# Kernel tuning notes

Measured on AMD Instinct MI355X. Metric: run time of the kernel, lower is better.

Reference implementation:

```python
import jax, jax.numpy as jnp
import numpy as np

B, D_IN, UNITS, H = 512, 1024, 1024, 8
K = V = UNITS // H  # key_dim = value_dim = head_dim = 128
P = 2 * H * K + H * V + 2 * H + UNITS  # total projection size = 4112


def setup_inputs() -> dict:
    key = jax.random.key(0)
    ks = jax.random.split(key, 7)
    return {
        "inputs": jax.random.normal(ks[0], (B, D_IN), jnp.float32),
        "h_tm1": jax.random.normal(ks[1], (B, UNITS), jnp.float32),
        "C_tm1": jax.random.normal(ks[2], (B, H * K * V), jnp.float32),
        "n_tm1": jax.random.uniform(ks[3], (B, H * K), jnp.float32),
        "kernel": jax.random.normal(ks[4], (D_IN, P), jnp.float32) / np.sqrt(D_IN),
        "recurrent_kernel": jax.random.normal(ks[5], (UNITS, P), jnp.float32) / np.sqrt(UNITS),
        "bias": jnp.zeros((P,), jnp.float32),
    }


def reference(inputs, h_tm1, C_tm1, n_tm1, kernel, recurrent_kernel, bias):
    b = inputs.shape[0]
    # fused input + recurrent projection: (b, P)
    proj = inputs @ kernel + bias + h_tm1 @ recurrent_kernel
    qs = H * K
    q = proj[:, :qs].reshape(b, H, K)
    k = proj[:, qs:2 * qs].reshape(b, H, K)
    v = proj[:, 2 * qs:2 * qs + H * V].reshape(b, H, V)
    i_g = jnp.exp(proj[:, 2 * qs + H * V:2 * qs + H * V + H])        # (b, H) exponential input gate
    f_g = jax.nn.sigmoid(proj[:, 2 * qs + H * V + H:2 * qs + H * V + 2 * H])  # (b, H)
    o_g = jax.nn.sigmoid(proj[:, -UNITS:])                            # (b, units)
    C = C_tm1.reshape(b, H, K, V)
    n = n_tm1.reshape(b, H, K)
    # covariance update: C_t = f*C + i*(k outer v)  -> (b, H, K, V)
    C_t = f_g[:, :, None, None] * C + i_g[:, :, None, None] * jnp.einsum('bhk,bhv->bhkv', k, v)
    # normalizer update: n_t = f*n + i*k
    n_t = f_g[:, :, None] * n + i_g[:, :, None] * k
    # readout: (C_t^T q) / (n_t . q)
    retr = jnp.einsum('bhkv,bhk->bhv', C_t, q)
    denom = jnp.sum(n_t * q, axis=-1, keepdims=True) + 1e-8
    h_t = o_g * (retr / denom).reshape(b, H * V)
    return h_t, C_t.reshape(b, H * K * V), n_t.reshape(b, H * K)
```

## Files before the change

kernel.cpp:

```cpp
#include <hip/hip_runtime.h>
#include <hip/hip_fp16.h>
#include <math.h>

#define NPROJ 4112
#define HOFF  0
#define COFF  524288
#define NOFF  67633152
#define SLICE 2105344
#define WTROWS 4160

using f16x8 = __attribute__((ext_vector_type(8))) _Float16;
using f32x4 = __attribute__((ext_vector_type(4))) float;

typedef __attribute__((address_space(1))) const ushort gu16;
typedef __attribute__((address_space(3))) ushort lu16;

#define ASCALE 64.0f
#define PSCALE (1.0 / 4096.0)

__device__ __forceinline__ void fp16_split(float x, ushort& h, ushort& l)
{
    const __half h1 = __float2half(x);
    h = __half_as_ushort(h1);
    l = __half_as_ushort(__float2half(x - __half2float(h1)));
}

__global__ __launch_bounds__(256)
void split_a2(const float* __restrict__ X0, const float* __restrict__ X1,
              ushort* __restrict__ Ah, ushort* __restrict__ Al)
{
    const int idx8 = (blockIdx.x * 256 + threadIdx.x) << 3;
    const int row = idx8 >> 11, k = idx8 & 2047;
    const float* src = (k < 1024) ? (X0 + (size_t)row * 1024 + k)
                                  : (X1 + (size_t)row * 1024 + (k - 1024));
    const float4 v0 = *(const float4*)src;
    const float4 v1 = *(const float4*)(src + 4);
    const float vv[8] = {v0.x, v0.y, v0.z, v0.w, v1.x, v1.y, v1.z, v1.w};
    ushort hh[8], ll[8];
#pragma unroll
    for (int i = 0; i < 8; ++i) fp16_split(vv[i] * ASCALE, hh[i], ll[i]);
    uint4 uh, ul;
    uh.x = hh[0] | ((unsigned)hh[1] << 16); uh.y = hh[2] | ((unsigned)hh[3] << 16);
    uh.z = hh[4] | ((unsigned)hh[5] << 16); uh.w = hh[6] | ((unsigned)hh[7] << 16);
    ul.x = ll[0] | ((unsigned)ll[1] << 16); ul.y = ll[2] | ((unsigned)ll[3] << 16);
    ul.z = ll[4] | ((unsigned)ll[5] << 16); ul.w = ll[6] | ((unsigned)ll[7] << 16);
    *(uint4*)(Ah + idx8) = uh;
    *(uint4*)(Al + idx8) = ul;
}

__global__ __launch_bounds__(256)
void split_w2(const float* __restrict__ W0, const float* __restrict__ W1,
              ushort* __restrict__ Wh, ushort* __restrict__ Wl)
{
    __shared__ __align__(16) ushort Th[64][72];
    __shared__ __align__(16) ushort Tl[64][72];
    const int t = threadIdx.x;
    const int kcat0 = blockIdx.x * 64;
    const int n0    = blockIdx.y * 64;
    const float* __restrict__ W = (kcat0 < 1024) ? W0 : W1;
    const int kbase = kcat0 & 1023;
    const int kr = t >> 4;
    const int nc = (t & 15) << 2;
    const bool ok = (n0 + nc) < NPROJ;
#pragma unroll
    for (int ii = 0; ii < 4; ++ii) {
        const int kl = kr + ii * 16;
        float4 w = make_float4(0.f, 0.f, 0.f, 0.f);
        if (ok) w = *(const float4*)(W + (size_t)(kbase + kl) * NPROJ + n0 + nc);
        const float x[4] = {w.x, w.y, w.z, w.w};
#pragma unroll
        for (int c = 0; c < 4; ++c) {
            ushort hh, ll;
            fp16_split(x[c] * ASCALE, hh, ll);
            Th[nc + c][kl] = hh;
            Tl[nc + c][kl] = ll;
        }
    }
    __syncthreads();
#pragma unroll
    for (int p = 0; p < 2; ++p) {
        const int c  = t + (p << 8);
        const int nn = c >> 3;
        const int kq = (c & 7) << 3;
        *(uint4*)(Wh + (size_t)(n0 + nn) * 2048 + kcat0 + kq) = *(uint4*)&Th[nn][kq];
        *(uint4*)(Wl + (size_t)(n0 + nn) * 2048 + kcat0 + kq) = *(uint4*)&Tl[nn][kq];
    }
}

__global__ __launch_bounds__(256)
void proj_mfma2(const ushort* __restrict__ Ah, const ushort* __restrict__ Al,
                const ushort* __restrict__ Wh, const ushort* __restrict__ Wl,
                float* __restrict__ pbuf)
{
    __shared__ __align__(16) ushort As[2][4096];
    __shared__ __align__(16) ushort Bs[2][4096];

    const int t    = threadIdx.x;
    const int col0 = blockIdx.x * 64;
    const int row0 = blockIdx.y * 64;
    const int z    = blockIdx.z;
    const int lane = t & 63, wid = t >> 6;
    const int wr = wid >> 1, wc = wid & 1;
    const int lr = lane & 15, lq = lane >> 4;

    const int r0s = t >> 3,        ch0 = t & 7;
    const int r1s = r0s + 32;
    const int so0 = (ch0 ^ (r0s & 7)) << 3;
    const int so1 = (ch0 ^ (r1s & 7)) << 3;
    const size_t kb = (size_t)z << 10;
    const size_t arow0 = (size_t)(row0 + r0s) * 2048 + kb;
    const size_t arow1 = (size_t)(row0 + r1s) * 2048 + kb;
    const size_t brow0 = (size_t)(col0 + r0s) * 2048 + kb;
    const size_t brow1 = (size_t)(col0 + r1s) * 2048 + kb;
    const int d0 = t << 3;
    const int d1 = d0 + 2048;

    int aoff[2][2], boff[2][2];
#pragma unroll
    for (int mi = 0; mi < 2; ++mi)
#pragma unroll
        for (int kh = 0; kh < 2; ++kh) {
            const int ra = (wr << 5) + (mi << 4) + lr;
            aoff[mi][kh] = ra * 64 + ((((kh << 2) + lq) ^ (ra & 7)) << 3);
            const int rb = (wc << 5) + (mi << 4) + lr;
            boff[mi][kh] = rb * 64 + ((((kh << 2) + lq) ^ (rb & 7)) << 3);
        }

    f32x4 acc[2][2] = {};

    for (int kt = 0; kt < 16; ++kt) {
        const int ko = kt << 6;
        __builtin_amdgcn_global_load_lds((gu16*)(Ah + arow0 + ko + so0), (lu16*)&As[0][d0], 16, 0, 0);
        __builtin_amdgcn_global_load_lds((gu16*)(Ah + arow1 + ko + so1), (lu16*)&As[0][d1], 16, 0, 0);
        __builtin_amdgcn_global_load_lds((gu16*)(Al + arow0 + ko + so0), (lu16*)&As[1][d0], 16, 0, 0);
        __builtin_amdgcn_global_load_lds((gu16*)(Al + arow1 + ko + so1), (lu16*)&As[1][d1], 16, 0, 0);
        __builtin_amdgcn_global_load_lds((gu16*)(Wh + brow0 + ko + so0), (lu16*)&Bs[0][d0], 16, 0, 0);
        __builtin_amdgcn_global_load_lds((gu16*)(Wh + brow1 + ko + so1), (lu16*)&Bs[0][d1], 16, 0, 0);
        __builtin_amdgcn_global_load_lds((gu16*)(Wl + brow0 + ko + so0), (lu16*)&Bs[1][d0], 16, 0, 0);
        __builtin_amdgcn_global_load_lds((gu16*)(Wl + brow1 + ko + so1), (lu16*)&Bs[1][d1], 16, 0, 0);
        __syncthreads();

#pragma unroll
        for (int kh = 0; kh < 2; ++kh) {
            f16x8 ah[2], al[2], bh[2], bl[2];
#pragma unroll
            for (int mi = 0; mi < 2; ++mi) {
                ah[mi] = *(const f16x8*)&As[0][aoff[mi][kh]];
                al[mi] = *(const f16x8*)&As[1][aoff[mi][kh]];
                bh[mi] = *(const f16x8*)&Bs[0][boff[mi][kh]];
                bl[mi] = *(const f16x8*)&Bs[1][boff[mi][kh]];
            }
#pragma unroll
            for (int mi = 0; mi < 2; ++mi)
#pragma unroll
                for (int ni = 0; ni < 2; ++ni) {
                    acc[mi][ni] = __builtin_amdgcn_mfma_f32_16x16x32_f16(ah[mi], bh[ni], acc[mi][ni], 0, 0, 0);
                    acc[mi][ni] = __builtin_amdgcn_mfma_f32_16x16x32_f16(ah[mi], bl[ni], acc[mi][ni], 0, 0, 0);
                    acc[mi][ni] = __builtin_amdgcn_mfma_f32_16x16x32_f16(al[mi], bh[ni], acc[mi][ni], 0, 0, 0);
                    acc[mi][ni] = __builtin_amdgcn_mfma_f32_16x16x32_f16(al[mi], bl[ni], acc[mi][ni], 0, 0, 0);
                }
        }
        __syncthreads();
    }

    float* __restrict__ dst = pbuf + (size_t)z * SLICE;
#pragma unroll
    for (int mi = 0; mi < 2; ++mi) {
        const int row = row0 + (wr << 5) + (mi << 4) + (lq << 2);
#pragma unroll
        for (int ni = 0; ni < 2; ++ni) {
            const int col = col0 + (wc << 5) + (ni << 4) + lr;
            if (col < NPROJ) {
#pragma unroll
                for (int j = 0; j < 4; ++j)
                    dst[(size_t)(row + j) * NPROJ + col] = acc[mi][ni][j];
            }
        }
    }
}

template<int NS>
__device__ __forceinline__ double psumN(const float* __restrict__ pb, size_t off,
                                        double pscale, float bv)
{
    double s = 0.0;
#pragma unroll
    for (int i = 0; i < NS; ++i) s += (double)pb[off + (size_t)i * SLICE];
    return s * pscale + (double)bv;
}

template<int NS>
__global__ __launch_bounds__(256)
void mlstm_update_fused(const float* __restrict__ pbuf, const float* __restrict__ bias,
                        const float* __restrict__ C_tm1, const float* __restrict__ n_tm1,
                        float* __restrict__ out, double pscale)
{
    const int bh = blockIdx.x;
    const int b  = bh >> 3;
    const int h  = bh & 7;
    const int t  = threadIdx.x;
    const size_t pb = (size_t)b * NPROJ;

    __shared__ double q_s[128];
    __shared__ double coef_s[128];
    __shared__ double prod_s[128];
    __shared__ double red_s[8][128];
    __shared__ double denom_s;

    const double ig = exp(psumN<NS>(pbuf, pb + 3072 + h, pscale, bias[3072 + h]));
    const double fg = 1.0 / (1.0 + exp(-psumN<NS>(pbuf, pb + 3080 + h, pscale, bias[3080 + h])));

    if (t < 128) {
        const double qv = psumN<NS>(pbuf, pb + h * 128 + t, pscale, bias[h * 128 + t]);
        const double kv = psumN<NS>(pbuf, pb + 1024 + h * 128 + t, pscale, bias[1024 + h * 128 + t]);
        q_s[t] = qv;
        const double cf = ig * kv;
        coef_s[t] = cf;
        const double nv = fma(fg, (double)n_tm1[(size_t)b * 1024 + h * 128 + t], cf);
        out[NOFF + (size_t)b * 1024 + h * 128 + t] = (float)nv;
        prod_s[t] = nv * qv;
    }
    __syncthreads();

    const int g = t >> 5;
    const int s = t & 31;
    const float4* __restrict__ Cin  = (const float4*)(C_tm1 + (size_t)bh * 16384);
    float4*       __restrict__ Cout = (float4*)(out + COFF + (size_t)bh * 16384);
    double v0, v1, v2, v3;
    {
        const size_t vo = pb + 2048 + h * 128 + (s << 2);
        const int    vb = 2048 + h * 128 + (s << 2);
        v0 = psumN<NS>(pbuf, vo + 0, pscale, bias[vb + 0]);
        v1 = psumN<NS>(pbuf, vo + 1, pscale, bias[vb + 1]);
        v2 = psumN<NS>(pbuf, vo + 2, pscale, bias[vb + 2]);
        v3 = psumN<NS>(pbuf, vo + 3, pscale, bias[vb + 3]);
    }

    double r0 = 0.0, r1 = 0.0, r2 = 0.0, r3 = 0.0;
#pragma unroll 4
    for (int it = 0; it < 16; ++it) {
        const int kr = (it << 3) + g;
        const float4 cc = Cin[(kr << 5) + s];
        const double cf = coef_s[kr];
        const double qv = q_s[kr];
        const double c0 = fma(fg, (double)cc.x, cf * v0);
        const double c1 = fma(fg, (double)cc.y, cf * v1);
        const double c2 = fma(fg, (double)cc.z, cf * v2);
        const double c3 = fma(fg, (double)cc.w, cf * v3);
        float4 cn;
        cn.x = (float)c0; cn.y = (float)c1; cn.z = (float)c2; cn.w = (float)c3;
        Cout[(kr << 5) + s] = cn;
        r0 = fma(c0, qv, r0);
        r1 = fma(c1, qv, r1);
        r2 = fma(c2, qv, r2);
        r3 = fma(c3, qv, r3);
    }
    red_s[g][(s << 2) + 0] = r0;
    red_s[g][(s << 2) + 1] = r1;
    red_s[g][(s << 2) + 2] = r2;
    red_s[g][(s << 2) + 3] = r3;
    __syncthreads();

    if (t < 64) {
        double x = prod_s[t] + prod_s[t + 64];
#pragma unroll
        for (int off = 32; off > 0; off >>= 1) x += __shfl_xor(x, off, 64);
        if (t == 0) denom_s = x + 1e-8;
    }
    __syncthreads();

    if (t < 32) {
        double r[4] = {0.0, 0.0, 0.0, 0.0};
#pragma unroll
        for (int gg = 0; gg < 8; ++gg) {
#pragma unroll
            for (int j = 0; j < 4; ++j) r[j] += red_s[gg][(t << 2) + j];
        }
        const double inv = 1.0 / denom_s;
        const size_t oo = pb + 3088 + h * 128 + (t << 2);
        const int    ob = 3088 + h * 128 + (t << 2);
        float4 hv;
        hv.x = (float)((1.0 / (1.0 + exp(-psumN<NS>(pbuf, oo + 0, pscale, bias[ob + 0])))) * (r[0] * inv));
        hv.y = (float)((1.0 / (1.0 + exp(-psumN<NS>(pbuf, oo + 1, pscale, bias[ob + 1])))) * (r[1] * inv));
        hv.z = (float)((1.0 / (1.0 + exp(-psumN<NS>(pbuf, oo + 2, pscale, bias[ob + 2])))) * (r[2] * inv));
        hv.w = (float)((1.0 / (1.0 + exp(-psumN<NS>(pbuf, oo + 3, pscale, bias[ob + 3])))) * (r[3] * inv));
        *(float4*)(out + HOFF + (size_t)b * 1024 + h * 128 + (t << 2)) = hv;
    }
}

__global__ __launch_bounds__(256)
void proj_gemm_sk(const float* __restrict__ X0, const float* __restrict__ X1,
                  const float* __restrict__ W0, const float* __restrict__ W1,
                  float* __restrict__ pbuf)
{
    const int K = 1024;
    const int N = NPROJ;
    __shared__ float As[32][68];
    __shared__ float Bs[32][68];

    const int tid  = threadIdx.x;
    const int row0 = blockIdx.y * 64;
    const int col0 = blockIdx.x * 64;
    const int z    = blockIdx.z;
    const float* __restrict__ A = (z < 2) ? X0 : X1;
    const float* __restrict__ W = (z < 2) ? W0 : W1;
    const int kbase = (z & 1) << 9;
    const int tx = tid & 15, ty = tid >> 4;

    const int ar = tid >> 2;
    const int aq = (tid & 3) << 2;
    const int bk = tid >> 4;
    const int bn = (tid & 15) << 2;
    const int gn = (col0 + bn < N) ? (col0 + bn) : (N - 4);
    const float* __restrict__ arow = A + (size_t)(row0 + ar) * K;

    float  acc32[4][4];
    double acc64[4][4];
#pragma unroll
    for (int i = 0; i < 4; ++i)
#pragma unroll
        for (int j = 0; j < 4; ++j) { acc32[i][j] = 0.f; acc64[i][j] = 0.0; }

    float4 pa0 = *(const float4*)(arow + kbase + aq);
    float4 pa1 = *(const float4*)(arow + kbase + aq + 16);
    float4 pb0 = *(const float4*)(W + (size_t)(kbase + bk) * N + gn);
    float4 pb1 = *(const float4*)(W + (size_t)(kbase + bk + 16) * N + gn);

    for (int kt = 0; kt < 16; ++kt) {
        As[aq + 0][ar] = pa0.x; As[aq + 1][ar] = pa0.y;
        As[aq + 2][ar] = pa0.z; As[aq + 3][ar] = pa0.w;
        As[aq + 16][ar] = pa1.x; As[aq + 17][ar] = pa1.y;
        As[aq + 18][ar] = pa1.z; As[aq + 19][ar] = pa1.w;
        *(float4*)&Bs[bk][bn]      = pb0;
        *(float4*)&Bs[bk + 16][bn] = pb1;
        __syncthreads();

        if (kt + 1 < 16) {
            const int k0n = kbase + ((kt + 1) << 5);
            pa0 = *(const float4*)(arow + k0n + aq);
            pa1 = *(const float4*)(arow + k0n + aq + 16);
            pb0 = *(const float4*)(W + (size_t)(k0n + bk) * N + gn);
            pb1 = *(const float4*)(W + (size_t)(k0n + bk + 16) * N + gn);
        }

#pragma unroll
        for (int kk = 0; kk < 32; ++kk) {
            const float4 av = *(const float4*)&As[kk][ty << 2];
            const float4 bv = *(const float4*)&Bs[kk][tx << 2];
            const float aa[4] = {av.x, av.y, av.z, av.w};
            const float bb[4] = {bv.x, bv.y, bv.z, bv.w};
#pragma unroll
            for (int i = 0; i < 4; ++i)
#pragma unroll
                for (int j = 0; j < 4; ++j)
                    acc32[i][j] = fmaf(aa[i], bb[j], acc32[i][j]);
        }
#pragma unroll
        for (int i = 0; i < 4; ++i)
#pragma unroll
            for (int j = 0; j < 4; ++j) {
                acc64[i][j] += (double)acc32[i][j];
                acc32[i][j] = 0.f;
            }
        __syncthreads();
    }

    float* __restrict__ dst = pbuf + (size_t)z * SLICE;
    const int c = col0 + (tx << 2);
    if (c < N) {
#pragma unroll
        for (int i = 0; i < 4; ++i) {
            const int row = row0 + (ty << 2) + i;
            float4 w;
            w.x = (float)acc64[i][0];
            w.y = (float)acc64[i][1];
            w.z = (float)acc64[i][2];
            w.w = (float)acc64[i][3];
            *(float4*)(dst + (size_t)row * N + c) = w;
        }
    }
}

__global__ __launch_bounds__(256)
void proj_gemm_fp32(const float* __restrict__ X0, const float* __restrict__ X1,
                    const float* __restrict__ W0, const float* __restrict__ W1,
                    const float* __restrict__ bias, float* __restrict__ proj)
{
    const int N = NPROJ;
    const int K = 1024;
    __shared__ float As[16][68];
    __shared__ float Bs[16][68];
    const int tid  = threadIdx.x;
    const int row0 = blockIdx.y * 64;
    const int col0 = blockIdx.x * 64;
    const int tx   = tid & 15;
    const int ty   = tid >> 4;
    float  acc32[4][4];
    double acc64[4][4];
#pragma unroll
    for (int i = 0; i < 4; ++i)
#pragma unroll
        for (int j = 0; j < 4; ++j) { acc32[i][j] = 0.f; acc64[i][j] = 0.0; }
    for (int src = 0; src < 2; ++src) {
        const float* __restrict__ A = src ? X1 : X0;
        const float* __restrict__ W = src ? W1 : W0;
        for (int kt = 0; kt < 64; ++kt) {
            const int k0 = kt << 4;
            {
                const int r  = tid >> 2;
                const int kq = (tid & 3) << 2;
                const float4 a = *(const float4*)(A + (size_t)(row0 + r) * K + k0 + kq);
                As[kq + 0][r] = a.x; As[kq + 1][r] = a.y;
                As[kq + 2][r] = a.z; As[kq + 3][r] = a.w;
            }
            {
                const int kr = tid >> 4;
                const int nc = (tid & 15) << 2;
                const int gn = col0 + nc;
                float4 bv = make_float4(0.f, 0.f, 0.f, 0.f);
                if (gn < N) bv = *(const float4*)(W + (size_t)(k0 + kr) * N + gn);
                *(float4*)&Bs[kr][nc] = bv;
            }
            __syncthreads();
#pragma unroll
            for (int kk = 0; kk < 16; ++kk) {
                const float4 av = *(const float4*)&As[kk][ty << 2];
                const float4 bv = *(const float4*)&Bs[kk][tx << 2];
                const float aa[4] = {av.x, av.y, av.z, av.w};
                const float bb[4] = {bv.x, bv.y, bv.z, bv.w};
#pragma unroll
                for (int i = 0; i < 4; ++i)
#pragma unroll
                    for (int j = 0; j < 4; ++j)
                        acc32[i][j] = fmaf(aa[i], bb[j], acc32[i][j]);
            }
            __syncthreads();
            if (kt & 1) {
#pragma unroll
                for (int i = 0; i < 4; ++i)
#pragma unroll
                    for (int j = 0; j < 4; ++j) {
                        acc64[i][j] += (double)acc32[i][j];
                        acc32[i][j] = 0.f;
                    }
            }
        }
    }
    const int c = col0 + (tx << 2);
    if (c < N) {
#pragma unroll
        for (int i = 0; i < 4; ++i) {
            const int row = row0 + (ty << 2) + i;
            float4 w;
            w.x = (float)(acc64[i][0] + (double)bias[c + 0]);
            w.y = (float)(acc64[i][1] + (double)bias[c + 1]);
            w.z = (float)(acc64[i][2] + (double)bias[c + 2]);
            w.w = (float)(acc64[i][3] + (double)bias[c + 3]);
            *(float4*)(proj + (size_t)row * N + c) = w;
        }
    }
}

__global__ __launch_bounds__(256)
void mlstm_update(const float* __restrict__ proj, const float* __restrict__ C_tm1,
                  const float* __restrict__ n_tm1, float* __restrict__ out)
{
    const int bh = blockIdx.x;
    const int b  = bh >> 3;
    const int h  = bh & 7;
    const int t  = threadIdx.x;
    const float* __restrict__ pr = proj + (size_t)b * NPROJ;

    __shared__ double q_s[128];
    __shared__ double coef_s[128];
    __shared__ double prod_s[128];
    __shared__ double red_s[8][128];
    __shared__ double denom_s;

    const double ig = exp((double)pr[3072 + h]);
    const double fg = 1.0 / (1.0 + exp(-(double)pr[3080 + h]));

    if (t < 128) {
        const double qv = (double)pr[h * 128 + t];
        const double kv = (double)pr[1024 + h * 128 + t];
        q_s[t] = qv;
        const double cf = ig * kv;
        coef_s[t] = cf;
        const double nv = fma(fg, (double)n_tm1[(size_t)b * 1024 + h * 128 + t], cf);
        out[NOFF + (size_t)b * 1024 + h * 128 + t] = (float)nv;
        prod_s[t] = nv * qv;
    }
    __syncthreads();

    const int g = t >> 5;
    const int s = t & 31;
    const float4* __restrict__ Cin  = (const float4*)(C_tm1 + (size_t)bh * 16384);
    float4*       __restrict__ Cout = (float4*)(out + COFF + (size_t)bh * 16384);
    const float4 vf = *(const float4*)(pr + 2048 + h * 128 + (s << 2));
    const double v0 = (double)vf.x, v1 = (double)vf.y, v2 = (double)vf.z, v3 = (double)vf.w;

    double r0 = 0.0, r1 = 0.0, r2 = 0.0, r3 = 0.0;
#pragma unroll 4
    for (int it = 0; it < 16; ++it) {
        const int kr = (it << 3) + g;
        const float4 cc = Cin[(kr << 5) + s];
        const double cf = coef_s[kr];
        const double qv = q_s[kr];
        const double c0 = fma(fg, (double)cc.x, cf * v0);
        const double c1 = fma(fg, (double)cc.y, cf * v1);
        const double c2 = fma(fg, (double)cc.z, cf * v2);
        const double c3 = fma(fg, (double)cc.w, cf * v3);
        float4 cn;
        cn.x = (float)c0; cn.y = (float)c1; cn.z = (float)c2; cn.w = (float)c3;
        Cout[(kr << 5) + s] = cn;
        r0 = fma(c0, qv, r0);
        r1 = fma(c1, qv, r1);
        r2 = fma(c2, qv, r2);
        r3 = fma(c3, qv, r3);
    }
    red_s[g][(s << 2) + 0] = r0;
    red_s[g][(s << 2) + 1] = r1;
    red_s[g][(s << 2) + 2] = r2;
    red_s[g][(s << 2) + 3] = r3;
    __syncthreads();

    if (t < 64) {
        double x = prod_s[t] + prod_s[t + 64];
#pragma unroll
        for (int off = 32; off > 0; off >>= 1) x += __shfl_xor(x, off, 64);
        if (t == 0) denom_s = x + 1e-8;
    }
    __syncthreads();

    if (t < 32) {
        double r[4] = {0.0, 0.0, 0.0, 0.0};
#pragma unroll
        for (int gg = 0; gg < 8; ++gg) {
#pragma unroll
            for (int j = 0; j < 4; ++j) r[j] += red_s[gg][(t << 2) + j];
        }
        const double inv = 1.0 / denom_s;
        const float* oo = pr + 3088 + h * 128 + (t << 2);
        float4 hv;
        hv.x = (float)((1.0 / (1.0 + exp(-(double)oo[0]))) * (r[0] * inv));
        hv.y = (float)((1.0 / (1.0 + exp(-(double)oo[1]))) * (r[1] * inv));
        hv.z = (float)((1.0 / (1.0 + exp(-(double)oo[2]))) * (r[2] * inv));
        hv.w = (float)((1.0 / (1.0 + exp(-(double)oo[3]))) * (r[3] * inv));
        *(float4*)(out + HOFF + (size_t)b * 1024 + h * 128 + (t << 2)) = hv;
    }
}

extern "C" void kernel_launch(void* const* d_in, const int* in_sizes, int n_in,
                              void* d_out, int out_size, void* d_ws, size_t ws_size,
                              hipStream_t stream)
{
    const float* inputs  = (const float*)d_in[0];
    const float* h_tm1   = (const float*)d_in[1];
    const float* C_tm1   = (const float*)d_in[2];
    const float* n_tm1   = (const float*)d_in[3];
    const float* kernelW = (const float*)d_in[4];
    const float* rkernel = (const float*)d_in[5];
    const float* bias    = (const float*)d_in[6];
    float* out = (float*)d_out;

    const size_t SZ_PB2 = (size_t)2 * SLICE * 4;
    const size_t SZ_A   = (size_t)512 * 2048 * 2;
    const size_t SZ_WT  = (size_t)WTROWS * 2048 * 2;
    const size_t OFF_AH = SZ_PB2;
    const size_t OFF_AL = OFF_AH + SZ_A;
    const size_t OFF_WH = OFF_AL + SZ_A;
    const size_t OFF_WL = OFF_WH + SZ_WT;
    const size_t NEED_MAIN = OFF_WL + SZ_WT;
    const size_t NEED_SK   = (size_t)4 * SLICE * 4;
    const size_t NEED_MIN  = (size_t)SLICE * 4;

    if (ws_size >= NEED_MAIN) {
        float*  pbuf = (float*)d_ws;
        ushort* Ah = (ushort*)((char*)d_ws + OFF_AH);
        ushort* Al = (ushort*)((char*)d_ws + OFF_AL);
        ushort* Wh = (ushort*)((char*)d_ws + OFF_WH);
        ushort* Wl = (ushort*)((char*)d_ws + OFF_WL);
        split_a2<<<dim3(512), dim3(256), 0, stream>>>(inputs, h_tm1, Ah, Al);
        split_w2<<<dim3(32, 65), dim3(256), 0, stream>>>(kernelW, rkernel, Wh, Wl);
        proj_mfma2<<<dim3(65, 8, 2), dim3(256), 0, stream>>>(Ah, Al, Wh, Wl, pbuf);
        mlstm_update_fused<2><<<dim3(4096), dim3(256), 0, stream>>>(pbuf, bias, C_tm1, n_tm1, out, PSCALE);
    } else if (ws_size >= NEED_SK) {
        float* pbuf = (float*)d_ws;
        proj_gemm_sk<<<dim3(65, 8, 4), dim3(256), 0, stream>>>(inputs, h_tm1, kernelW, rkernel, pbuf);
        mlstm_update_fused<4><<<dim3(4096), dim3(256), 0, stream>>>(pbuf, bias, C_tm1, n_tm1, out, 1.0);
    } else if (ws_size >= NEED_MIN) {
        float* proj = (float*)d_ws;
        proj_gemm_fp32<<<dim3(65, 8), dim3(256), 0, stream>>>(inputs, h_tm1, kernelW, rkernel, bias, proj);
        mlstm_update<<<dim3(4096), dim3(256), 0, stream>>>(proj, C_tm1, n_tm1, out);
    }
}
```

Baseline: 183.2 us.

## Double-buffer projection GEMM tiles, shrink K-step, drop low-low split product

```diff
diff --git a/kernel.cpp b/kernel.cpp
--- a/kernel.cpp
+++ b/kernel.cpp
@@ -88,7 +88,7 @@
 }
 
 __global__ __launch_bounds__(256)
-void proj_mfma2(const ushort* __restrict__ Ah, const ushort* __restrict__ Al,
+void proj_mfma3(const ushort* __restrict__ Ah, const ushort* __restrict__ Al,
                 const ushort* __restrict__ Wh, const ushort* __restrict__ Wl,
                 float* __restrict__ pbuf)
 {
@@ -103,65 +103,59 @@
     const int wr = wid >> 1, wc = wid & 1;
     const int lr = lane & 15, lq = lane >> 4;
 
-    const int r0s = t >> 3,        ch0 = t & 7;
-    const int r1s = r0s + 32;
-    const int so0 = (ch0 ^ (r0s & 7)) << 3;
-    const int so1 = (ch0 ^ (r1s & 7)) << 3;
+    const int rs = t >> 2, js = t & 3;
+    const int cs = (js + (rs >> 1)) & 3;
     const size_t kb = (size_t)z << 10;
-    const size_t arow0 = (size_t)(row0 + r0s) * 2048 + kb;
-    const size_t arow1 = (size_t)(row0 + r1s) * 2048 + kb;
-    const size_t brow0 = (size_t)(col0 + r0s) * 2048 + kb;
-    const size_t brow1 = (size_t)(col0 + r1s) * 2048 + kb;
-    const int d0 = t << 3;
-    const int d1 = d0 + 2048;
-
-    int aoff[2][2], boff[2][2];
-#pragma unroll
-    for (int mi = 0; mi < 2; ++mi)
-#pragma unroll
-        for (int kh = 0; kh < 2; ++kh) {
-            const int ra = (wr << 5) + (mi << 4) + lr;
-            aoff[mi][kh] = ra * 64 + ((((kh << 2) + lq) ^ (ra & 7)) << 3);
-            const int rb = (wc << 5) + (mi << 4) + lr;
-            boff[mi][kh] = rb * 64 + ((((kh << 2) + lq) ^ (rb & 7)) << 3);
-        }
+    const size_t arow = (size_t)(row0 + rs) * 2048 + kb + (cs << 3);
+    const size_t brow = (size_t)(col0 + rs) * 2048 + kb + (cs << 3);
+    const int d0 = t << 3, d1 = d0 + 2048;
+
+#define STG(BUF, KT)                                                                         \
+    {                                                                                        \
+        const int ko = (KT) << 5;                                                            \
+        __builtin_amdgcn_global_load_lds((gu16*)(Ah + arow + ko), (lu16*)&As[BUF][d0], 16, 0, 0); \
+        __builtin_amdgcn_global_load_lds((gu16*)(Al + arow + ko), (lu16*)&As[BUF][d1], 16, 0, 0); \
+        __builtin_amdgcn_global_load_lds((gu16*)(Wh + brow + ko), (lu16*)&Bs[BUF][d0], 16, 0, 0); \
+        __builtin_amdgcn_global_load_lds((gu16*)(Wl + brow + ko), (lu16*)&Bs[BUF][d1], 16, 0, 0); \
+    }
+
+    int aoff[2], boff[2];
+#pragma unroll
+    for (int mi = 0; mi < 2; ++mi) {
+        const int ra = (wr << 5) + (mi << 4) + lr;
+        aoff[mi] = (ra << 5) + (((lq - (ra >> 1)) & 3) << 3);
+        const int rb = (wc << 5) + (mi << 4) + lr;
+        boff[mi] = (rb << 5) + (((lq - (rb >> 1)) & 3) << 3);
+    }
 
     f32x4 acc[2][2] = {};
 
-    for (int kt = 0; kt < 16; ++kt) {
-        const int ko = kt << 6;
-        __builtin_amdgcn_global_load_lds((gu16*)(Ah + arow0 + ko + so0), (lu16*)&As[0][d0], 16, 0, 0);
-        __builtin_amdgcn_global_load_lds((gu16*)(Ah + arow1 + ko + so1), (lu16*)&As[0][d1], 16, 0, 0);
-        __builtin_amdgcn_global_load_lds((gu16*)(Al + arow0 + ko + so0), (lu16*)&As[1][d0], 16, 0, 0);
-        __builtin_amdgcn_global_load_lds((gu16*)(Al + arow1 + ko + so1), (lu16*)&As[1][d1], 16, 0, 0);
-        __builtin_amdgcn_global_load_lds((gu16*)(Wh + brow0 + ko + so0), (lu16*)&Bs[0][d0], 16, 0, 0);
-        __builtin_amdgcn_global_load_lds((gu16*)(Wh + brow1 + ko + so1), (lu16*)&Bs[0][d1], 16, 0, 0);
-        __builtin_amdgcn_global_load_lds((gu16*)(Wl + brow0 + ko + so0), (lu16*)&Bs[1][d0], 16, 0, 0);
-        __builtin_amdgcn_global_load_lds((gu16*)(Wl + brow1 + ko + so1), (lu16*)&Bs[1][d1], 16, 0, 0);
+    STG(0, 0)
+    __syncthreads();
+
+    for (int kt = 0; kt < 32; ++kt) {
+        const int cur = kt & 1;
+        if (kt + 1 < 32) STG(cur ^ 1, kt + 1)
+
+        f16x8 ah[2], al[2], bh[2], bl[2];
+#pragma unroll
+        for (int mi = 0; mi < 2; ++mi) {
+            ah[mi] = *(const f16x8*)&As[cur][aoff[mi]];
+            al[mi] = *(const f16x8*)&As[cur][2048 + aoff[mi]];
+            bh[mi] = *(const f16x8*)&Bs[cur][boff[mi]];
+            bl[mi] = *(const f16x8*)&Bs[cur][2048 + boff[mi]];
+        }
+#pragma unroll
+        for (int mi = 0; mi < 2; ++mi)
+#pragma unroll
+            for (int ni = 0; ni < 2; ++ni) {
+                acc[mi][ni] = __builtin_amdgcn_mfma_f32_16x16x32_f16(ah[mi], bh[ni], acc[mi][ni], 0, 0, 0);
+                acc[mi][ni] = __builtin_amdgcn_mfma_f32_16x16x32_f16(ah[mi], bl[ni], acc[mi][ni], 0, 0, 0);
+                acc[mi][ni] = __builtin_amdgcn_mfma_f32_16x16x32_f16(al[mi], bh[ni], acc[mi][ni], 0, 0, 0);
+            }
         __syncthreads();
-
-#pragma unroll
-        for (int kh = 0; kh < 2; ++kh) {
-            f16x8 ah[2], al[2], bh[2], bl[2];
-#pragma unroll
-            for (int mi = 0; mi < 2; ++mi) {
-                ah[mi] = *(const f16x8*)&As[0][aoff[mi][kh]];
-                al[mi] = *(const f16x8*)&As[1][aoff[mi][kh]];
-                bh[mi] = *(const f16x8*)&Bs[0][boff[mi][kh]];
-                bl[mi] = *(const f16x8*)&Bs[1][boff[mi][kh]];
-            }
-#pragma unroll
-            for (int mi = 0; mi < 2; ++mi)
-#pragma unroll
-                for (int ni = 0; ni < 2; ++ni) {
-                    acc[mi][ni] = __builtin_amdgcn_mfma_f32_16x16x32_f16(ah[mi], bh[ni], acc[mi][ni], 0, 0, 0);
-                    acc[mi][ni] = __builtin_amdgcn_mfma_f32_16x16x32_f16(ah[mi], bl[ni], acc[mi][ni], 0, 0, 0);
-                    acc[mi][ni] = __builtin_amdgcn_mfma_f32_16x16x32_f16(al[mi], bh[ni], acc[mi][ni], 0, 0, 0);
-                    acc[mi][ni] = __builtin_amdgcn_mfma_f32_16x16x32_f16(al[mi], bl[ni], acc[mi][ni], 0, 0, 0);
-                }
-        }
-        __syncthreads();
-    }
+    }
+#undef STG
 
     float* __restrict__ dst = pbuf + (size_t)z * SLICE;
 #pragma unroll
@@ -582,7 +576,7 @@
         ushort* Wl = (ushort*)((char*)d_ws + OFF_WL);
         split_a2<<<dim3(512), dim3(256), 0, stream>>>(inputs, h_tm1, Ah, Al);
         split_w2<<<dim3(32, 65), dim3(256), 0, stream>>>(kernelW, rkernel, Wh, Wl);
-        proj_mfma2<<<dim3(65, 8, 2), dim3(256), 0, stream>>>(Ah, Al, Wh, Wl, pbuf);
+        proj_mfma3<<<dim3(65, 8, 2), dim3(256), 0, stream>>>(Ah, Al, Wh, Wl, pbuf);
         mlstm_update_fused<2><<<dim3(4096), dim3(256), 0, stream>>>(pbuf, bias, C_tm1, n_tm1, out, PSCALE);
     } else if (ws_size >= NEED_SK) {
         float* pbuf = (float*)d_ws;
```

Measured after the change: 192.8 us. +5.2%, slower.

## Double-buffer split-fp16 GEMM, drop lo*lo term, handle gate columns separately

Applied to the files above, without the earlier changes.

```diff
diff --git a/kernel.cpp b/kernel.cpp
--- a/kernel.cpp
+++ b/kernel.cpp
@@ -7,7 +7,6 @@
 #define COFF  524288
 #define NOFF  67633152
 #define SLICE 2105344
-#define WTROWS 4160
 
 using f16x8 = __attribute__((ext_vector_type(8))) _Float16;
 using f32x4 = __attribute__((ext_vector_type(4))) float;
@@ -61,12 +60,10 @@
     const int kbase = kcat0 & 1023;
     const int kr = t >> 4;
     const int nc = (t & 15) << 2;
-    const bool ok = (n0 + nc) < NPROJ;
 #pragma unroll
     for (int ii = 0; ii < 4; ++ii) {
         const int kl = kr + ii * 16;
-        float4 w = make_float4(0.f, 0.f, 0.f, 0.f);
-        if (ok) w = *(const float4*)(W + (size_t)(kbase + kl) * NPROJ + n0 + nc);
+        const float4 w = *(const float4*)(W + (size_t)(kbase + kl) * NPROJ + n0 + nc);
         const float x[4] = {w.x, w.y, w.z, w.w};
 #pragma unroll
         for (int c = 0; c < 4; ++c) {
@@ -88,12 +85,12 @@
 }
 
 __global__ __launch_bounds__(256)
-void proj_mfma2(const ushort* __restrict__ Ah, const ushort* __restrict__ Al,
+void proj_mfma4(const ushort* __restrict__ Ah, const ushort* __restrict__ Al,
                 const ushort* __restrict__ Wh, const ushort* __restrict__ Wl,
                 float* __restrict__ pbuf)
 {
-    __shared__ __align__(16) ushort As[2][4096];
-    __shared__ __align__(16) ushort Bs[2][4096];
+    __shared__ __align__(16) ushort As[2][2][4096];
+    __shared__ __align__(16) ushort Bs[2][2][4096];
 
     const int t    = threadIdx.x;
     const int col0 = blockIdx.x * 64;
@@ -103,7 +100,7 @@
     const int wr = wid >> 1, wc = wid & 1;
     const int lr = lane & 15, lq = lane >> 4;
 
-    const int r0s = t >> 3,        ch0 = t & 7;
+    const int r0s = t >> 3, ch0 = t & 7;
     const int r1s = r0s + 32;
     const int so0 = (ch0 ^ (r0s & 7)) << 3;
     const int so1 = (ch0 ^ (r1s & 7)) << 3;
@@ -112,8 +109,20 @@
     const size_t arow1 = (size_t)(row0 + r1s) * 2048 + kb;
     const size_t brow0 = (size_t)(col0 + r0s) * 2048 + kb;
     const size_t brow1 = (size_t)(col0 + r1s) * 2048 + kb;
-    const int d0 = t << 3;
-    const int d1 = d0 + 2048;
+    const int d0 = t << 3, d1 = d0 + 2048;
+
+#define STG4(BUF, KT)                                                                             \
+    {                                                                                             \
+        const int ko = (KT) << 6;                                                                 \
+        __builtin_amdgcn_global_load_lds((gu16*)(Ah + arow0 + ko + so0), (lu16*)&As[BUF][0][d0], 16, 0, 0); \
+        __builtin_amdgcn_global_load_lds((gu16*)(Ah + arow1 + ko + so1), (lu16*)&As[BUF][0][d1], 16, 0, 0); \
+        __builtin_amdgcn_global_load_lds((gu16*)(Al + arow0 + ko + so0), (lu16*)&As[BUF][1][d0], 16, 0, 0); \
+        __builtin_amdgcn_global_load_lds((gu16*)(Al + arow1 + ko + so1), (lu16*)&As[BUF][1][d1], 16, 0, 0); \
+        __builtin_amdgcn_global_load_lds((gu16*)(Wh + brow0 + ko + so0), (lu16*)&Bs[BUF][0][d0], 16, 0, 0); \
+        __builtin_amdgcn_global_load_lds((gu16*)(Wh + brow1 + ko + so1), (lu16*)&Bs[BUF][0][d1], 16, 0, 0); \
+        __builtin_amdgcn_global_load_lds((gu16*)(Wl + brow0 + ko + so0), (lu16*)&Bs[BUF][1][d0], 16, 0, 0); \
+        __builtin_amdgcn_global_load_lds((gu16*)(Wl + brow1 + ko + so1), (lu16*)&Bs[BUF][1][d1], 16, 0, 0); \
+    }
 
     int aoff[2][2], boff[2][2];
 #pragma unroll
@@ -121,34 +130,29 @@
 #pragma unroll
         for (int kh = 0; kh < 2; ++kh) {
             const int ra = (wr << 5) + (mi << 4) + lr;
-            aoff[mi][kh] = ra * 64 + ((((kh << 2) + lq) ^ (ra & 7)) << 3);
+            aoff[mi][kh] = (ra << 6) + ((((kh << 2) + lq) ^ (ra & 7)) << 3);
             const int rb = (wc << 5) + (mi << 4) + lr;
-            boff[mi][kh] = rb * 64 + ((((kh << 2) + lq) ^ (rb & 7)) << 3);
+            boff[mi][kh] = (rb << 6) + ((((kh << 2) + lq) ^ (rb & 7)) << 3);
         }
 
     f32x4 acc[2][2] = {};
 
+    STG4(0, 0)
+    __syncthreads();
+
     for (int kt = 0; kt < 16; ++kt) {
-        const int ko = kt << 6;
-        __builtin_amdgcn_global_load_lds((gu16*)(Ah + arow0 + ko + so0), (lu16*)&As[0][d0], 16, 0, 0);
-        __builtin_amdgcn_global_load_lds((gu16*)(Ah + arow1 + ko + so1), (lu16*)&As[0][d1], 16, 0, 0);
-        __builtin_amdgcn_global_load_lds((gu16*)(Al + arow0 + ko + so0), (lu16*)&As[1][d0], 16, 0, 0);
-        __builtin_amdgcn_global_load_lds((gu16*)(Al + arow1 + ko + so1), (lu16*)&As[1][d1], 16, 0, 0);
-        __builtin_amdgcn_global_load_lds((gu16*)(Wh + brow0 + ko + so0), (lu16*)&Bs[0][d0], 16, 0, 0);
-        __builtin_amdgcn_global_load_lds((gu16*)(Wh + brow1 + ko + so1), (lu16*)&Bs[0][d1], 16, 0, 0);
-        __builtin_amdgcn_global_load_lds((gu16*)(Wl + brow0 + ko + so0), (lu16*)&Bs[1][d0], 16, 0, 0);
-        __builtin_amdgcn_global_load_lds((gu16*)(Wl + brow1 + ko + so1), (lu16*)&Bs[1][d1], 16, 0, 0);
-        __syncthreads();
+        const int cur = kt & 1;
+        if (kt + 1 < 16) STG4(cur ^ 1, kt + 1)
 
 #pragma unroll
         for (int kh = 0; kh < 2; ++kh) {
             f16x8 ah[2], al[2], bh[2], bl[2];
 #pragma unroll
             for (int mi = 0; mi < 2; ++mi) {
-                ah[mi] = *(const f16x8*)&As[0][aoff[mi][kh]];
-                al[mi] = *(const f16x8*)&As[1][aoff[mi][kh]];
-                bh[mi] = *(const f16x8*)&Bs[0][boff[mi][kh]];
-                bl[mi] = *(const f16x8*)&Bs[1][boff[mi][kh]];
+                ah[mi] = *(const f16x8*)&As[cur][0][aoff[mi][kh]];
+                al[mi] = *(const f16x8*)&As[cur][1][aoff[mi][kh]];
+                bh[mi] = *(const f16x8*)&Bs[cur][0][boff[mi][kh]];
+                bl[mi] = *(const f16x8*)&Bs[cur][1][boff[mi][kh]];
             }
 #pragma unroll
             for (int mi = 0; mi < 2; ++mi)
@@ -157,11 +161,11 @@
                     acc[mi][ni] = __builtin_amdgcn_mfma_f32_16x16x32_f16(ah[mi], bh[ni], acc[mi][ni], 0, 0, 0);
                     acc[mi][ni] = __builtin_amdgcn_mfma_f32_16x16x32_f16(ah[mi], bl[ni], acc[mi][ni], 0, 0, 0);
                     acc[mi][ni] = __builtin_amdgcn_mfma_f32_16x16x32_f16(al[mi], bh[ni], acc[mi][ni], 0, 0, 0);
-                    acc[mi][ni] = __builtin_amdgcn_mfma_f32_16x16x32_f16(al[mi], bl[ni], acc[mi][ni], 0, 0, 0);
                 }
         }
         __syncthreads();
     }
+#undef STG4
 
     float* __restrict__ dst = pbuf + (size_t)z * SLICE;
 #pragma unroll
@@ -170,12 +174,43 @@
 #pragma unroll
         for (int ni = 0; ni < 2; ++ni) {
             const int col = col0 + (wc << 5) + (ni << 4) + lr;
-            if (col < NPROJ) {
-#pragma unroll
-                for (int j = 0; j < 4; ++j)
-                    dst[(size_t)(row + j) * NPROJ + col] = acc[mi][ni][j];
-            }
-        }
+#pragma unroll
+            for (int j = 0; j < 4; ++j)
+                dst[(size_t)(row + j) * NPROJ + col] = acc[mi][ni][j];
+        }
+    }
+}
+
+__global__ __launch_bounds__(256)
+void proj_tail4(const float* __restrict__ X0, const float* __restrict__ X1,
+                const float* __restrict__ W0, const float* __restrict__ W1,
+                float* __restrict__ pbuf)
+{
+    const int t = threadIdx.x;
+    const int o = (blockIdx.x << 6) + (t >> 2);
+    const int q = t & 3;
+    const int row = o >> 4;
+    const int col = 4096 + (o & 15);
+    const float* __restrict__ X = (q >> 1) ? X1 : X0;
+    const float* __restrict__ W = (q >> 1) ? W1 : W0;
+    const int kb = (q & 1) << 9;
+    const float* __restrict__ xr = X + (size_t)row * 1024 + kb;
+    const float* __restrict__ wc = W + (size_t)kb * NPROJ + col;
+    float s0 = 0.f, s1 = 0.f, s2 = 0.f, s3 = 0.f;
+#pragma unroll 8
+    for (int k = 0; k < 512; k += 4) {
+        const float4 xv = *(const float4*)(xr + k);
+        s0 = fmaf(xv.x, wc[(size_t)(k + 0) * NPROJ], s0);
+        s1 = fmaf(xv.y, wc[(size_t)(k + 1) * NPROJ], s1);
+        s2 = fmaf(xv.z, wc[(size_t)(k + 2) * NPROJ], s2);
+        s3 = fmaf(xv.w, wc[(size_t)(k + 3) * NPROJ], s3);
+    }
+    double r = (double)((s0 + s1) + (s2 + s3));
+    r += __shfl_xor(r, 1, 64);
+    r += __shfl_xor(r, 2, 64);
+    if (q == 0) {
+        pbuf[(size_t)row * NPROJ + col] = (float)(r * 4096.0);
+        pbuf[SLICE + (size_t)row * NPROJ + col] = 0.0f;
     }
 }
 
@@ -565,7 +600,7 @@
 
     const size_t SZ_PB2 = (size_t)2 * SLICE * 4;
     const size_t SZ_A   = (size_t)512 * 2048 * 2;
-    const size_t SZ_WT  = (size_t)WTROWS * 2048 * 2;
+    const size_t SZ_WT  = (size_t)4096 * 2048 * 2;
     const size_t OFF_AH = SZ_PB2;
     const size_t OFF_AL = OFF_AH + SZ_A;
     const size_t OFF_WH = OFF_AL + SZ_A;
@@ -581,8 +616,9 @@
         ushort* Wh = (ushort*)((char*)d_ws + OFF_WH);
         ushort* Wl = (ushort*)((char*)d_ws + OFF_WL);
         split_a2<<<dim3(512), dim3(256), 0, stream>>>(inputs, h_tm1, Ah, Al);
-        split_w2<<<dim3(32, 65), dim3(256), 0, stream>>>(kernelW, rkernel, Wh, Wl);
-        proj_mfma2<<<dim3(65, 8, 2), dim3(256), 0, stream>>>(Ah, Al, Wh, Wl, pbuf);
+        split_w2<<<dim3(32, 64), dim3(256), 0, stream>>>(kernelW, rkernel, Wh, Wl);
+        proj_mfma4<<<dim3(64, 8, 2), dim3(256), 0, stream>>>(Ah, Al, Wh, Wl, pbuf);
+        proj_tail4<<<dim3(128), dim3(256), 0, stream>>>(inputs, h_tm1, kernelW, rkernel, pbuf);
         mlstm_update_fused<2><<<dim3(4096), dim3(256), 0, stream>>>(pbuf, bias, C_tm1, n_tm1, out, PSCALE);
     } else if (ws_size >= NEED_SK) {
         float* pbuf = (float*)d_ws;
```

Result: slower. 209.3 us (+14.3%).
